# Kernel tuning notes

Measured on AMD Instinct MI355X. Metric: run time of the kernel, lower is better.

Reference implementation:

```python
import jax, jax.numpy as jnp
import numpy as np

B = 2            # batch
T = 1_000_000    # texels per texture
C = 16           # channels
G = 500_000      # flattened groups
K = 9            # texels per group (mesh-neighborhood stencil)


def setup_inputs() -> dict:
    key = jax.random.key(0)
    k1, k2, k3 = jax.random.split(key, 3)
    mesh_ids = jax.random.randint(k1, (B,), 0, 4, dtype=jnp.int32)
    textures = jax.random.normal(k2, (B, T, C), dtype=jnp.float32)
    group_idx = jax.random.randint(k3, (G, K), 0, T, dtype=jnp.int32)
    return {"mesh_ids": mesh_ids, "textures": textures, "group_idx": group_idx}


def reference(mesh_ids, textures, group_idx):
    # Forward pass of textures_to_flattened_groups: gather per-texel features
    # into flattened mesh-connectivity groups.
    # textures: [B, T, C]; group_idx: [G, K] -> out: [B, G, K, C]
    out = jnp.take(textures, group_idx.reshape(-1), axis=1)  # [B, G*K, C]
    return out.reshape(textures.shape[0], G, K, textures.shape[-1])
```

## Files before the change

kernel.cpp:

```cpp
#include <hip/hip_runtime.h>


typedef float f4 __attribute__((ext_vector_type(4)));

constexpr long long T_ = 1000000;
constexpr int       C4 = 4;
constexpr long long GK = 500000LL * 9;
constexpr long long PACKED_F4 = T_ * 2 * C4;

__global__ __launch_bounds__(256) void
TMSCNN_repack_kernel(const f4* __restrict__ textures, f4* __restrict__ packed)
{
    const unsigned tid = blockIdx.x * blockDim.x + threadIdx.x;
    if (tid >= (unsigned)PACKED_F4) return;
    const unsigned j   = tid & 7;
    const unsigned t   = tid >> 3;
    const unsigned b   = j >> 2;
    const unsigned c4  = j & 3;
    const long long src = ((long long)b * T_ + (long long)t) * C4 + c4;
    packed[tid] = textures[src];
}

__global__ __launch_bounds__(256) void
TMSCNN_gather_kernel(const f4* __restrict__ packed,
                     const int* __restrict__ group_idx,
                     f4*       __restrict__ out)
{
    const unsigned tid = blockIdx.x * blockDim.x + threadIdx.x;
    if (tid >= (unsigned)(GK * 8)) return;
    const unsigned j   = tid & 7;
    const unsigned gk  = tid >> 3;
    const unsigned b   = j >> 2;
    const unsigned c4  = j & 3;

    const int idx = __builtin_nontemporal_load(&group_idx[gk]);

    const f4 v = packed[(long long)idx * 8 + j];

    const long long dst = (long long)b * (GK * C4) + (long long)gk * C4 + c4;
    __builtin_nontemporal_store(v, &out[dst]);
}

__global__ __launch_bounds__(256) void
TMSCNN_direct_kernel(const f4* __restrict__ textures,
                     const int* __restrict__ group_idx,
                     f4*       __restrict__ out)
{
    const unsigned tid = blockIdx.x * blockDim.x + threadIdx.x;
    if (tid >= (unsigned)(GK * C4)) return;
    const int          c4 = tid & 3;
    const unsigned int gk = tid >> 2;

    const int idx = group_idx[gk];
    const long long src0 = (long long)idx * C4 + c4;
    const long long src1 = (T_ + (long long)idx) * C4 + c4;
    const f4 v0 = textures[src0];
    const f4 v1 = textures[src1];
    const long long dst0 = (long long)gk * C4 + c4;
    const long long dst1 = (GK + (long long)gk) * C4 + c4;
    __builtin_nontemporal_store(v0, &out[dst0]);
    __builtin_nontemporal_store(v1, &out[dst1]);
}

extern "C" void kernel_launch(void* const* d_in, const int* in_sizes, int n_in,
                              void* d_out, int out_size, void* d_ws, size_t ws_size,
                              hipStream_t stream) {
    const f4*  textures  = (const f4*)d_in[1];
    const int* group_idx = (const int*)d_in[2];
    f4*        out       = (f4*)d_out;

    const int threads = 256;
    const size_t packed_bytes = (size_t)PACKED_F4 * sizeof(f4);

    if (d_ws != nullptr && ws_size >= packed_bytes) {
        f4* packed = (f4*)d_ws;

        const long long nA = PACKED_F4;
        const long long nB = GK * 8;

        TMSCNN_repack_kernel<<<(int)((nA + threads - 1) / threads), threads, 0, stream>>>(
            textures, packed);
        TMSCNN_gather_kernel<<<(int)((nB + threads - 1) / threads), threads, 0, stream>>>(
            packed, group_idx, out);
    } else {
        const unsigned long long total = (unsigned long long)GK * C4;
        TMSCNN_direct_kernel<<<(int)((total + threads - 1) / threads), threads, 0, stream>>>(
            textures, group_idx, out);
    }
}
```

Before: 758.4 us.

## Use output buffer tail as scratch for packed textures when no workspace

When no workspace is available, the fallback no longer uses a direct gather. It repacks the textures into an interleaved batch layout stored in the tail of the output buffer. It then gathers in stages, ordered so the scratch region is read before it is overwritten: a full interleaved gather for the first groups, a batch-0 gather for the rest, and a final batch-1 gather that reads the original textures. The aim is coalesced 128-byte packed reads in the fallback path, at the cost of extra kernel launches and an aliasing scheme that depends on launch order.

```diff
diff --git a/kernel.cpp b/kernel.cpp
--- a/kernel.cpp
+++ b/kernel.cpp
@@ -3,38 +3,41 @@
 
 typedef float f4 __attribute__((ext_vector_type(4)));
 
-constexpr long long T_ = 1000000;
-constexpr int       C4 = 4;
-constexpr long long GK = 500000LL * 9;
+constexpr long long T_  = 1000000;
+constexpr int       C4  = 4;
+constexpr long long GK  = 500000LL * 9;
 constexpr long long PACKED_F4 = T_ * 2 * C4;
+constexpr long long OUT_F4    = 2 * GK * C4;
+constexpr long long SCRATCH_OFF_F4 = OUT_F4 - PACKED_F4;
+constexpr long long GK_SPLIT = 2500000;
 
 __global__ __launch_bounds__(256) void
 TMSCNN_repack_kernel(const f4* __restrict__ textures, f4* __restrict__ packed)
 {
     const unsigned tid = blockIdx.x * blockDim.x + threadIdx.x;
     if (tid >= (unsigned)PACKED_F4) return;
-    const unsigned j   = tid & 7;
-    const unsigned t   = tid >> 3;
-    const unsigned b   = j >> 2;
-    const unsigned c4  = j & 3;
+    const unsigned j  = tid & 7;
+    const unsigned t  = tid >> 3;
+    const unsigned b  = j >> 2;
+    const unsigned c4 = j & 3;
     const long long src = ((long long)b * T_ + (long long)t) * C4 + c4;
     packed[tid] = textures[src];
 }
 
 __global__ __launch_bounds__(256) void
-TMSCNN_gather_kernel(const f4* __restrict__ packed,
-                     const int* __restrict__ group_idx,
-                     f4*       __restrict__ out)
+TMSCNN_gather_full_kernel(const f4* __restrict__ packed,
+                          const int* __restrict__ group_idx,
+                          f4*       __restrict__ out,
+                          unsigned long long n)
 {
     const unsigned tid = blockIdx.x * blockDim.x + threadIdx.x;
-    if (tid >= (unsigned)(GK * 8)) return;
-    const unsigned j   = tid & 7;
-    const unsigned gk  = tid >> 3;
-    const unsigned b   = j >> 2;
-    const unsigned c4  = j & 3;
+    if (tid >= n) return;
+    const unsigned j  = tid & 7;
+    const unsigned gk = tid >> 3;
+    const unsigned b  = j >> 2;
+    const unsigned c4 = j & 3;
 
     const int idx = __builtin_nontemporal_load(&group_idx[gk]);
-
     const f4 v = packed[(long long)idx * 8 + j];
 
     const long long dst = (long long)b * (GK * C4) + (long long)gk * C4 + c4;
@@ -42,24 +45,37 @@
 }
 
 __global__ __launch_bounds__(256) void
-TMSCNN_direct_kernel(const f4* __restrict__ textures,
-                     const int* __restrict__ group_idx,
-                     f4*       __restrict__ out)
+TMSCNN_gather_b0_kernel(const f4* __restrict__ packed,
+                        const int* __restrict__ group_idx,
+                        f4*       __restrict__ out)
 {
     const unsigned tid = blockIdx.x * blockDim.x + threadIdx.x;
-    if (tid >= (unsigned)(GK * C4)) return;
-    const int          c4 = tid & 3;
-    const unsigned int gk = tid >> 2;
+    if (tid >= (unsigned)((GK - GK_SPLIT) * C4)) return;
+    const unsigned c4 = tid & 3;
+    const long long gk = GK_SPLIT + (long long)(tid >> 2);
 
-    const int idx = group_idx[gk];
-    const long long src0 = (long long)idx * C4 + c4;
-    const long long src1 = (T_ + (long long)idx) * C4 + c4;
-    const f4 v0 = textures[src0];
-    const f4 v1 = textures[src1];
-    const long long dst0 = (long long)gk * C4 + c4;
-    const long long dst1 = (GK + (long long)gk) * C4 + c4;
-    __builtin_nontemporal_store(v0, &out[dst0]);
-    __builtin_nontemporal_store(v1, &out[dst1]);
+    const int idx = __builtin_nontemporal_load(&group_idx[gk]);
+    const f4 v = packed[(long long)idx * 8 + c4];
+
+    const long long dst = gk * C4 + c4;
+    __builtin_nontemporal_store(v, &out[dst]);
+}
+
+__global__ __launch_bounds__(256) void
+TMSCNN_gather_tail_kernel(const f4* __restrict__ textures,
+                          const int* __restrict__ group_idx,
+                          f4*       __restrict__ out)
+{
+    const unsigned tid = blockIdx.x * blockDim.x + threadIdx.x;
+    if (tid >= (unsigned)((GK - GK_SPLIT) * C4)) return;
+    const unsigned c4 = tid & 3;
+    const long long gk = GK_SPLIT + (long long)(tid >> 2);
+
+    const int idx = __builtin_nontemporal_load(&group_idx[gk]);
+    const f4 v = textures[(T_ + (long long)idx) * C4 + c4];
+
+    const long long dst = GK * C4 + gk * C4 + c4;
+    __builtin_nontemporal_store(v, &out[dst]);
 }
 
 extern "C" void kernel_launch(void* const* d_in, const int* in_sizes, int n_in,
@@ -74,17 +90,26 @@
 
     if (d_ws != nullptr && ws_size >= packed_bytes) {
         f4* packed = (f4*)d_ws;
+        TMSCNN_repack_kernel<<<(int)(PACKED_F4 / threads), threads, 0, stream>>>(
+            textures, packed);
+        const unsigned long long nB = (unsigned long long)GK * 8;
+        TMSCNN_gather_full_kernel<<<(int)(nB / threads), threads, 0, stream>>>(
+            packed, group_idx, out, nB);
+    } else {
+        f4* packed = out + SCRATCH_OFF_F4;
 
-        const long long nA = PACKED_F4;
-        const long long nB = GK * 8;
+        TMSCNN_repack_kernel<<<(int)(PACKED_F4 / threads), threads, 0, stream>>>(
+            textures, packed);
 
-        TMSCNN_repack_kernel<<<(int)((nA + threads - 1) / threads), threads, 0, stream>>>(
-            textures, packed);
-        TMSCNN_gather_kernel<<<(int)((nB + threads - 1) / threads), threads, 0, stream>>>(
+        const unsigned long long n2a = (unsigned long long)GK_SPLIT * 8;
+        TMSCNN_gather_full_kernel<<<(int)(n2a / threads), threads, 0, stream>>>(
+            packed, group_idx, out, n2a);
+
+        const long long n2b = (GK - GK_SPLIT) * C4;
+        TMSCNN_gather_b0_kernel<<<(int)(n2b / threads), threads, 0, stream>>>(
             packed, group_idx, out);
-    } else {
-        const unsigned long long total = (unsigned long long)GK * C4;
-        TMSCNN_direct_kernel<<<(int)((total + threads - 1) / threads), threads, 0, stream>>>(
+
+        TMSCNN_gather_tail_kernel<<<(int)(n2b / threads), threads, 0, stream>>>(
             textures, group_idx, out);
     }
 }
```

New measurement: 756.8 us. About the same (-0.2%).
